# Kernel optimization log

Hardware: AMD Instinct MI355X
Metric: run time of the kernel (lower is better)

The kernel has to match this reference:

```python
import jax, jax.numpy as jnp
import numpy as np

B, T, N, M, D = 4, 64, 32, 32, 128  # batch, time, price points, liquidity points, feature dim


def setup_inputs() -> dict:
    key = jax.random.key(0)
    ks = jax.random.split(key, 6)
    w = lambda k, shape: jax.random.normal(k, shape, jnp.float32) * 0.05
    return {
        "price": jax.random.normal(ks[0], (B, T, N, D), jnp.float32),
        "liquid": jax.random.normal(ks[1], (B, T, M, D), jnp.float32),
        "W_p": w(ks[2], (D, D)), "b_p": jnp.zeros((D,), jnp.float32),
        "W_v": w(ks[3], (D, D)), "b_v": jnp.zeros((D,), jnp.float32),
        "W1": w(ks[4], (4 * D, D)), "b1": jnp.zeros((D,), jnp.float32),
        "W2": w(ks[5], (D, D)), "b2": jnp.zeros((D,), jnp.float32),
    }


def reference(price, liquid, W_p, b_p, W_v, b_v, W1, b1, W2, b2):
    # proj_p / proj_v
    p = price @ W_p + b_p    # [B, T, N, D]
    v = liquid @ W_v + b_v   # [B, T, M, D]
    p4 = p[:, :, :, None, :]  # [B, T, N, 1, D]
    v4 = v[:, :, None, :, :]  # [B, T, 1, M, D]
    prod = p4 * v4            # [B, T, N, M, D]
    absdiff = jnp.abs(p4 - v4)
    full = (p.shape[0], p.shape[1], p.shape[2], v.shape[2], p.shape[3])
    pair = jnp.concatenate(
        [jnp.broadcast_to(p4, full), jnp.broadcast_to(v4, full), prod, absdiff],
        axis=-1,
    )  # [B, T, N, M, 4D]
    h = jax.nn.silu(pair @ W1 + b1)  # [B, T, N, M, D]
    grid = h @ W2 + b2               # [B, T, N, M, D]
    return grid.reshape(grid.shape[0], grid.shape[1], grid.shape[2] * grid.shape[3], grid.shape[4])
```

## Files before the change

### kernel.cpp

```cpp
#include <hip/hip_runtime.h>


typedef short  short8  __attribute__((ext_vector_type(8)));
typedef float  f32x4   __attribute__((ext_vector_type(4)));
typedef float  f32x16  __attribute__((ext_vector_type(16)));

#define DEV static __device__ __forceinline__

DEV float bf2f(unsigned short h) {
  unsigned u = ((unsigned)h) << 16;
  float f;
  __builtin_memcpy(&f, &u, 4);
  return f;
}
DEV unsigned short f2bf(float f) {
  unsigned u;
  __builtin_memcpy(&u, &f, 4);
  unsigned r = (u + 0x7FFFu + ((u >> 16) & 1u)) >> 16;
  return (unsigned short)r;
}
DEV unsigned pk2(float fh, float fl) {
  return __builtin_amdgcn_perm(__float_as_uint(fh), __float_as_uint(fl), 0x07060302u);
}
DEV float lo16(unsigned u) { return __uint_as_float(u << 16); }
DEV float hi16(unsigned u) { return __uint_as_float(u & 0xFFFF0000u); }

union V8 { uint4 u; unsigned a[4]; short8 s; };

__global__ void k0_prep(const float* __restrict__ Wp, const float* __restrict__ bp,
                        const float* __restrict__ Wv, const float* __restrict__ bv,
                        const float* __restrict__ W1, const float* __restrict__ b1,
                        const float* __restrict__ W2,
                        unsigned short* __restrict__ w1cd, unsigned short* __restrict__ w2sw,
                        unsigned short* __restrict__ wpsw, unsigned short* __restrict__ gpsw,
                        unsigned short* __restrict__ wvsw, unsigned short* __restrict__ gvsw,
                        float* __restrict__ c1) {
  int t = blockIdx.x * 256 + threadIdx.x;
  if (t < 32768) {
    int j = t & 7, lane = (t >> 3) & 63, r2 = t >> 9;
    int ct = r2 & 3, kt = r2 >> 2;
    int k = kt * 16 + (lane >> 5) * 8 + j;
    int c = ct * 32 + (lane & 31);
    w1cd[t] = f2bf(W1[(256 + k) * 128 + c]);
  } else if (t < 114688) {
    int e = t - 32768;
    int sec = e >> 14;
    int f = e & 16383;
    int j = f & 7, lane = (f >> 3) & 63, r2 = f >> 9;
    if (sec == 0) {
      int ct = r2 & 3, kt = r2 >> 2;
      int k = kt * 16 + (lane >> 5) * 8 + j;
      int c = ct * 32 + (lane & 31);
      w2sw[f] = f2bf(W2[k * 128 + c]);
    } else {
      int kt = r2 & 3, ct = r2 >> 2;
      int k = kt * 32 + ((lane >> 4) & 3) * 8 + j;
      int n = ct * 16 + (lane & 15);
      if (sec == 1) {
        wpsw[f] = f2bf(Wp[k * 128 + n]);
      } else if (sec == 2) {
        float s = 0.f;
        for (int e2 = 0; e2 < 128; e2++) s += Wp[k * 128 + e2] * W1[e2 * 128 + n];
        gpsw[f] = f2bf(s);
      } else if (sec == 3) {
        wvsw[f] = f2bf(Wv[k * 128 + n]);
      } else {
        float s = 0.f;
        for (int e2 = 0; e2 < 128; e2++) s += Wv[k * 128 + e2] * W1[(128 + e2) * 128 + n];
        gvsw[f] = f2bf(s);
      }
    }
  } else if (t < 114816) {
    int c = t - 114688;
    float s = b1[c];
    for (int e2 = 0; e2 < 128; e2++)
      s += bp[e2] * W1[e2 * 128 + c] + bv[e2] * W1[(128 + e2) * 128 + c];
    c1[c] = s;
  }
}

__global__ __launch_bounds__(256, 2) void k1_proj(
    const float* __restrict__ price, const float* __restrict__ liquid,
    const float* __restrict__ bp, const float* __restrict__ bv, const float* __restrict__ c1,
    const unsigned short* __restrict__ wpsw, const unsigned short* __restrict__ gpsw,
    const unsigned short* __restrict__ wvsw, const unsigned short* __restrict__ gvsw,
    unsigned short* __restrict__ pbf, unsigned short* __restrict__ vbf,
    float* __restrict__ pAc, unsigned short* __restrict__ vbsw) {
  __shared__ __align__(16) unsigned short sA[128 * 136];
  int b = blockIdx.x;
  int chunk = b >> 2, sel = b & 3;
  int side = sel >> 1, half = sel & 1;
  int rowbase = chunk * 128;
  const float* src = side ? liquid : price;
  const unsigned short* bsw = side ? (half ? gvsw : wvsw) : (half ? gpsw : wpsw);
  int tid = threadIdx.x;

#pragma unroll
  for (int i = 0; i < 16; i++) {
    int e4 = i * 256 + tid;
    int row = e4 >> 5, c4 = (e4 & 31) * 4;
    float4 f = *(const float4*)(src + (rowbase + row) * 128 + c4);
    uint2 pk;
    pk.x = pk2(f.y, f.x);
    pk.y = pk2(f.w, f.z);
    *(uint2*)&sA[row * 136 + c4] = pk;
  }
  __syncthreads();

  int lane = tid & 63, w = tid >> 6;
  int l15 = lane & 15, q4 = lane >> 4;
  f32x4 acc[2][8] = {};
#pragma unroll
  for (int kt = 0; kt < 4; kt++) {
    short8 a0 = *(const short8*)&sA[(w * 32 + l15) * 136 + kt * 32 + q4 * 8];
    short8 a1 = *(const short8*)&sA[(w * 32 + 16 + l15) * 136 + kt * 32 + q4 * 8];
#pragma unroll
    for (int ct = 0; ct < 8; ct++) {
      short8 bfr = *(const short8*)(bsw + ((ct * 4 + kt) * 64 + lane) * 8);
      acc[0][ct] = __builtin_amdgcn_mfma_f32_16x16x32_bf16(a0, bfr, acc[0][ct], 0, 0, 0);
      acc[1][ct] = __builtin_amdgcn_mfma_f32_16x16x32_bf16(a1, bfr, acc[1][ct], 0, 0, 0);
    }
  }

#pragma unroll
  for (int rg = 0; rg < 2; rg++) {
#pragma unroll
    for (int ct = 0; ct < 8; ct++) {
      int col = ct * 16 + l15;
      int lrow0 = w * 32 + rg * 16 + q4 * 4;
#pragma unroll
      for (int ri = 0; ri < 4; ri++) {
        int grow = rowbase + lrow0 + ri;
        float val = acc[rg][ct][ri];
        if (side == 0) {
          if (half == 0) pbf[grow * 128 + col] = f2bf(val + bp[col]);
          else           pAc[grow * 128 + col] = val + c1[col];
        } else {
          if (half == 0) vbf[grow * 128 + col] = f2bf(val + bv[col]);
          else {
            int btl = grow >> 5, m = grow & 31;
            int idx = btl * 4096 +
                      ((((m >> 4) * 4 + (col >> 5)) * 64) + ((m >> 3) & 1) * 32 + (col & 31)) * 8 +
                      (m & 7);
            vbsw[idx] = f2bf(val);
          }
        }
      }
    }
  }
}

__global__ __launch_bounds__(256, 3) void k2_fused(
    const unsigned short* __restrict__ pbf, const unsigned short* __restrict__ vbf,
    const float* __restrict__ pAc, const unsigned short* __restrict__ w1cd,
    const unsigned short* __restrict__ vbsw, const unsigned short* __restrict__ w2sw,
    const float* __restrict__ b2, float* __restrict__ out) {
  __shared__ __align__(16) unsigned short sVf[4096];
  __shared__ __align__(16) unsigned short sP[4 * 136];
  __shared__ __align__(16) unsigned short sHt[4][32 * 72];
  int bt = blockIdx.x >> 3, slab = (blockIdx.x & 7) * 4;
  int tid = threadIdx.x;

  if (tid < 64) {
    int row = tid >> 4, seg = tid & 15;
    *(uint4*)&sP[row * 136 + seg * 8] = *(const uint4*)(pbf + (bt * 32 + slab + row) * 128 + seg * 8);
  }
#pragma unroll
  for (int g2 = 0; g2 < 2; g2++) {
    int g = tid * 2 + g2;
    int m = g & 31, k0 = (g >> 5) * 8;
    *(uint4*)&sVf[g * 8] = *(const uint4*)(vbf + (bt * 32 + m) * 128 + k0);
  }
  __syncthreads();

  int lane = tid & 63, w = tid >> 6;
  int m31 = lane & 31, hi = lane >> 5;
  int n = slab + w;
  const unsigned short* vbswt = vbsw + bt * 4096;

  float pa[4], bia[4];
#pragma unroll
  for (int ct = 0; ct < 4; ct++) {
    pa[ct]  = pAc[(bt * 32 + n) * 128 + ct * 32 + m31];
    bia[ct] = b2[ct * 32 + m31];
  }

  f32x16 acc[4] = {};

#pragma unroll
  for (int kt = 0; kt < 8; kt++) {
    V8 vf, pp, x, y;
    vf.u = *(const uint4*)&sVf[((kt * 2 + hi) * 32 + m31) * 8];
    pp.u = *(const uint4*)&sP[w * 136 + kt * 16 + hi * 8];
#pragma unroll
    for (int i = 0; i < 4; i++) {
      float vl = lo16(vf.a[i]), vh = hi16(vf.a[i]);
      float al = lo16(pp.a[i]), ah = hi16(pp.a[i]);
      x.a[i] = pk2(ah * vh, al * vl);
      y.a[i] = pk2(fabsf(ah - vh), fabsf(al - vl));
    }
    const unsigned short* bxb = w1cd + (kt * 4) * 512;
    const unsigned short* byb = w1cd + ((kt + 8) * 4) * 512;
#pragma unroll
    for (int ct = 0; ct < 4; ct++) {
      short8 bx = *(const short8*)(bxb + ct * 512 + lane * 8);
      short8 by = *(const short8*)(byb + ct * 512 + lane * 8);
      acc[ct] = __builtin_amdgcn_mfma_f32_32x32x16_bf16(x.s, bx, acc[ct], 0, 0, 0);
      acc[ct] = __builtin_amdgcn_mfma_f32_32x32x16_bf16(y.s, by, acc[ct], 0, 0, 0);
    }
  }

#pragma unroll
  for (int kt2 = 0; kt2 < 2; kt2++) {
    short8 indf;
#pragma unroll
    for (int j = 0; j < 8; j++)
      indf[j] = (short)(((kt2 * 16 + hi * 8 + j) == m31) ? 0x3F80 : 0);
#pragma unroll
    for (int ct = 0; ct < 4; ct++) {
      short8 bi = *(const short8*)(vbswt + (kt2 * 4 + ct) * 512 + lane * 8);
      acc[ct] = __builtin_amdgcn_mfma_f32_32x32x16_bf16(indf, bi, acc[ct], 0, 0, 0);
    }
  }

  unsigned short* sh = &sHt[w][0];
  f32x16 o[4] = {};
#pragma unroll
  for (int p = 0; p < 2; p++) {
#pragma unroll
    for (int c2 = 0; c2 < 2; c2++) {
      int ct = p * 2 + c2;
#pragma unroll
      for (int reg = 0; reg < 16; reg++) {
        float z = acc[ct][reg] + pa[ct];
        float hv = z * __builtin_amdgcn_rcpf(1.f + __expf(-z));
        int mr = (reg & 3) + 8 * (reg >> 2) + 4 * hi;
        sh[mr * 72 + c2 * 32 + m31] = (unsigned short)(__float_as_uint(hv) >> 16);
      }
    }
#pragma unroll
    for (int kt = 0; kt < 4; kt++) {
      int ktg = p * 4 + kt;
      short8 hf = *(const short8*)&sh[m31 * 72 + kt * 16 + hi * 8];
#pragma unroll
      for (int ct2 = 0; ct2 < 4; ct2++) {
        short8 wf = *(const short8*)(w2sw + ((ktg * 4 + ct2) * 64 + lane) * 8);
        o[ct2] = __builtin_amdgcn_mfma_f32_32x32x16_bf16(hf, wf, o[ct2], 0, 0, 0);
      }
    }
  }

  int rowb = bt * 1024 + n * 32;
#pragma unroll
  for (int ct2 = 0; ct2 < 4; ct2++) {
#pragma unroll
    for (int reg = 0; reg < 16; reg++) {
      int mr = (reg & 3) + 8 * (reg >> 2) + 4 * hi;
      out[(rowb + mr) * 128 + ct2 * 32 + m31] = o[ct2][reg] + bia[ct2];
    }
  }
}

extern "C" void kernel_launch(void* const* d_in, const int* in_sizes, int n_in,
                              void* d_out, int out_size, void* d_ws, size_t ws_size,
                              hipStream_t stream) {
  const float* price  = (const float*)d_in[0];
  const float* liquid = (const float*)d_in[1];
  const float* Wp     = (const float*)d_in[2];
  const float* bp     = (const float*)d_in[3];
  const float* Wv     = (const float*)d_in[4];
  const float* bv     = (const float*)d_in[5];
  const float* W1     = (const float*)d_in[6];
  const float* b1     = (const float*)d_in[7];
  const float* W2     = (const float*)d_in[8];
  const float* b2     = (const float*)d_in[9];

  char* ws = (char*)d_ws;
  unsigned short* w1cd = (unsigned short*)(ws + 0);
  unsigned short* w2sw = (unsigned short*)(ws + 65536);
  unsigned short* wpsw = (unsigned short*)(ws + 98304);
  unsigned short* gpsw = (unsigned short*)(ws + 131072);
  unsigned short* wvsw = (unsigned short*)(ws + 163840);
  unsigned short* gvsw = (unsigned short*)(ws + 196608);
  float*          c1   = (float*)(ws + 229376);
  unsigned short* pbf  = (unsigned short*)(ws + 262144);
  unsigned short* vbf  = (unsigned short*)(ws + 2359296);
  float*          pAc  = (float*)(ws + 4456448);
  unsigned short* vbsw = (unsigned short*)(ws + 8650752);

  hipLaunchKernelGGL(k0_prep, dim3(449), dim3(256), 0, stream,
                     Wp, bp, Wv, bv, W1, b1, W2, w1cd, w2sw, wpsw, gpsw, wvsw, gvsw, c1);
  hipLaunchKernelGGL(k1_proj, dim3(256), dim3(256), 0, stream,
                     price, liquid, bp, bv, c1, wpsw, gpsw, wvsw, gvsw, pbf, vbf, pAc, vbsw);
  hipLaunchKernelGGL(k2_fused, dim3(2048), dim3(256), 0, stream,
                     pbf, vbf, pAc, w1cd, vbsw, w2sw, b2, (float*)d_out);
}
```

Measured before the change: 213.7 us.

## Stage W1, V-bias and W2 tiles in LDS via async global_load_lds

The fused kernel previously read W1, the per-(b,t) V-bias term and W2 fragments straight from global memory inside the MFMA loops. It now copies them into LDS with global_load_lds. W1 uses a double buffer prefetched one k-step ahead, and W2 is staged into LDS regions freed by earlier phases. The goal is to take global-load latency off the MFMA critical path and share weight tiles across the block's four waves. In exchange it adds a __syncthreads every k-step, raises LDS use per block (which may limit occupancy), and switches output writes to nontemporal stores.

```diff
diff --git a/kernel.cpp b/kernel.cpp
--- a/kernel.cpp
+++ b/kernel.cpp
@@ -24,6 +24,12 @@
 }
 DEV float lo16(unsigned u) { return __uint_as_float(u << 16); }
 DEV float hi16(unsigned u) { return __uint_as_float(u & 0xFFFF0000u); }
+
+DEV void cp16(unsigned short* l, const unsigned short* g) {
+  __builtin_amdgcn_global_load_lds(
+      (const __attribute__((address_space(1))) unsigned int*)g,
+      (__attribute__((address_space(3))) unsigned int*)l, 16, 0, 0);
+}
 
 union V8 { uint4 u; unsigned a[4]; short8 s; };
 
@@ -158,8 +164,16 @@
   __shared__ __align__(16) unsigned short sVf[4096];
   __shared__ __align__(16) unsigned short sP[4 * 136];
   __shared__ __align__(16) unsigned short sHt[4][32 * 72];
+  __shared__ __align__(16) unsigned short sVb[4096];
+  __shared__ __align__(16) unsigned short sT[8192];
   int bt = blockIdx.x >> 3, slab = (blockIdx.x & 7) * 4;
   int tid = threadIdx.x;
+  const unsigned short* vbswt = vbsw + bt * 4096;
+
+  cp16(&sT[tid * 8],        w1cd + tid * 8);
+  cp16(&sT[2048 + tid * 8], w1cd + 16384 + tid * 8);
+  cp16(&sVb[tid * 8],        vbswt + tid * 8);
+  cp16(&sVb[2048 + tid * 8], vbswt + 2048 + tid * 8);
 
   if (tid < 64) {
     int row = tid >> 4, seg = tid & 15;
@@ -176,7 +190,6 @@
   int lane = tid & 63, w = tid >> 6;
   int m31 = lane & 31, hi = lane >> 5;
   int n = slab + w;
-  const unsigned short* vbswt = vbsw + bt * 4096;
 
   float pa[4], bia[4];
 #pragma unroll
@@ -189,6 +202,12 @@
 
 #pragma unroll
   for (int kt = 0; kt < 8; kt++) {
+    const unsigned short* bcur = sT + (kt & 1) * 4096;
+    if (kt < 7) {
+      unsigned short* bnx = sT + ((kt + 1) & 1) * 4096;
+      cp16(&bnx[tid * 8],        w1cd + (kt + 1) * 2048 + tid * 8);
+      cp16(&bnx[2048 + tid * 8], w1cd + (kt + 9) * 2048 + tid * 8);
+    }
     V8 vf, pp, x, y;
     vf.u = *(const uint4*)&sVf[((kt * 2 + hi) * 32 + m31) * 8];
     pp.u = *(const uint4*)&sP[w * 136 + kt * 16 + hi * 8];
@@ -199,16 +218,19 @@
       x.a[i] = pk2(ah * vh, al * vl);
       y.a[i] = pk2(fabsf(ah - vh), fabsf(al - vl));
     }
-    const unsigned short* bxb = w1cd + (kt * 4) * 512;
-    const unsigned short* byb = w1cd + ((kt + 8) * 4) * 512;
 #pragma unroll
     for (int ct = 0; ct < 4; ct++) {
-      short8 bx = *(const short8*)(bxb + ct * 512 + lane * 8);
-      short8 by = *(const short8*)(byb + ct * 512 + lane * 8);
+      short8 bx = *(const short8*)(bcur + ct * 512 + lane * 8);
+      short8 by = *(const short8*)(bcur + 2048 + ct * 512 + lane * 8);
       acc[ct] = __builtin_amdgcn_mfma_f32_32x32x16_bf16(x.s, bx, acc[ct], 0, 0, 0);
       acc[ct] = __builtin_amdgcn_mfma_f32_32x32x16_bf16(y.s, by, acc[ct], 0, 0, 0);
     }
-  }
+    __syncthreads();
+  }
+
+#pragma unroll
+  for (int r = 0; r < 4; r++)
+    cp16(&sT[r * 2048 + tid * 8], w2sw + r * 2048 + tid * 8);
 
 #pragma unroll
   for (int kt2 = 0; kt2 < 2; kt2++) {
@@ -218,15 +240,22 @@
       indf[j] = (short)(((kt2 * 16 + hi * 8 + j) == m31) ? 0x3F80 : 0);
 #pragma unroll
     for (int ct = 0; ct < 4; ct++) {
-      short8 bi = *(const short8*)(vbswt + (kt2 * 4 + ct) * 512 + lane * 8);
+      short8 bi = *(const short8*)(sVb + (kt2 * 4 + ct) * 512 + lane * 8);
       acc[ct] = __builtin_amdgcn_mfma_f32_32x32x16_bf16(indf, bi, acc[ct], 0, 0, 0);
     }
   }
+  __syncthreads();
 
   unsigned short* sh = &sHt[w][0];
   f32x16 o[4] = {};
 #pragma unroll
   for (int p = 0; p < 2; p++) {
+    if (p == 0) {
+#pragma unroll
+      for (int r = 0; r < 4; r++)
+        cp16(r < 2 ? &sVf[r * 2048 + tid * 8] : &sVb[(r - 2) * 2048 + tid * 8],
+             w2sw + 8192 + r * 2048 + tid * 8);
+    }
 #pragma unroll
     for (int c2 = 0; c2 < 2; c2++) {
       int ct = p * 2 + c2;
@@ -240,14 +269,19 @@
     }
 #pragma unroll
     for (int kt = 0; kt < 4; kt++) {
-      int ktg = p * 4 + kt;
       short8 hf = *(const short8*)&sh[m31 * 72 + kt * 16 + hi * 8];
 #pragma unroll
       for (int ct2 = 0; ct2 < 4; ct2++) {
-        short8 wf = *(const short8*)(w2sw + ((ktg * 4 + ct2) * 64 + lane) * 8);
+        int idx = (kt * 4 + ct2) * 512 + lane * 8;
+        const unsigned short* wsrc;
+        if (p == 0)       wsrc = sT + idx;
+        else if (kt < 2)  wsrc = sVf + idx;
+        else              wsrc = sVb + idx - 4096;
+        short8 wf = *(const short8*)wsrc;
         o[ct2] = __builtin_amdgcn_mfma_f32_32x32x16_bf16(hf, wf, o[ct2], 0, 0, 0);
       }
     }
+    if (p == 0) __syncthreads();
   }
 
   int rowb = bt * 1024 + n * 32;
@@ -256,7 +290,8 @@
 #pragma unroll
     for (int reg = 0; reg < 16; reg++) {
       int mr = (reg & 3) + 8 * (reg >> 2) + 4 * hi;
-      out[(rowb + mr) * 128 + ct2 * 32 + m31] = o[ct2][reg] + bia[ct2];
+      __builtin_nontemporal_store(o[ct2][reg] + bia[ct2],
+                                  &out[(rowb + mr) * 128 + ct2 * 32 + m31]);
     }
   }
 }
```

Result: no change. 210.5 us (-1.5%).
